# Performance work log

Measured on AMD Instinct MI355X. Metric: run time of the kernel, lower is better.

Reference implementation:

```python
import jax, jax.numpy as jnp
import numpy as np

N = 50000      # nodes
E = 500000     # edges (includes N self-loops)
DIN = 512
DOUT = 256
NEG_SLOPE = 0.01  # torch nn.LeakyReLU default


def setup_inputs() -> dict:
    key = jax.random.key(0)
    k1, k2, k3, k4, k5 = jax.random.split(key, 5)
    x = jax.random.normal(k1, (N, DIN), dtype=jnp.float32)
    # xavier_normal_ with gain=1.414
    std_W = 1.414 * np.sqrt(2.0 / (DIN + DOUT))
    W = jax.random.normal(k2, (DIN, DOUT), dtype=jnp.float32) * std_W
    std_a = 1.414 * np.sqrt(2.0 / (1 + 2 * DOUT))
    a = jax.random.normal(k3, (2 * DOUT,), dtype=jnp.float32) * std_a
    # first N edges are self-loops so every row-sum is nonzero
    loops = jnp.arange(N, dtype=jnp.int32)
    edge_src = jnp.concatenate([loops, jax.random.randint(k4, (E - N,), 0, N, dtype=jnp.int32)])
    edge_dst = jnp.concatenate([loops, jax.random.randint(k5, (E - N,), 0, N, dtype=jnp.int32)])
    return {"x": x, "W": W, "a": a, "edge_src": edge_src, "edge_dst": edge_dst}


def reference(x, W, a, edge_src, edge_dst):
    n = x.shape[0]
    d = W.shape[1]
    h = x @ W  # [N, DOUT]
    # a . [h_src ; h_dst] decomposed per-node, then gathered per-edge
    s_src = h @ a[:d]   # [N]
    s_dst = h @ a[d:]   # [N]
    score = s_src[edge_src] + s_dst[edge_dst]          # [E]
    e = jnp.exp(-jax.nn.leaky_relu(score, NEG_SLOPE))  # [E]
    # sparse softmax denominator: spmm(edge, e, ones) == segment sum over src
    e_rowsum = jax.ops.segment_sum(e, edge_src, num_segments=n)            # [N]
    # numerator: spmm(edge, e, h) == sum_j e_ij * h_j per row i
    h_prime = jax.ops.segment_sum(e[:, None] * h[edge_dst], edge_src, num_segments=n)  # [N, DOUT]
    h_prime = h_prime / e_rowsum[:, None]
    return jax.nn.elu(h_prime)  # concat=True branch
```

## Files before the change

kernel.cpp:

```cpp
#include <hip/hip_runtime.h>
#include <math.h>

#define DIN 512
#define DOUT 256
#define NEG_SLOPE 0.01f
#define BM 128
#define BK 32

typedef __attribute__((ext_vector_type(8))) short bf16x8;
typedef __attribute__((ext_vector_type(4))) float f32x4;
typedef __attribute__((ext_vector_type(4))) unsigned int u32x4;

__device__ __forceinline__ unsigned short f2bf(float f) {
    unsigned int u = __float_as_uint(f);
    unsigned int r = (u + 0x7FFFu + ((u >> 16) & 1u)) >> 16;
    return (unsigned short)r;
}
__device__ __forceinline__ float bf2f(unsigned short u) {
    return __uint_as_float(((unsigned int)u) << 16);
}
__device__ __forceinline__ unsigned int cvtpk(float lo, float hi) {
    unsigned int r;
    asm("v_cvt_pk_bf16_f32 %0, %1, %2" : "=v"(r) : "v"(lo), "v"(hi));
    return r;
}
__device__ __forceinline__ void gload16(const void* g, void* l) {
    __builtin_amdgcn_global_load_lds(
        (const __attribute__((address_space(1))) void*)g,
        (__attribute__((address_space(3))) void*)l, 16, 0, 0);
}

__global__ void wt_convert(const float* __restrict__ W, unsigned short* __restrict__ Wt) {
    int t = blockIdx.x * blockDim.x + threadIdx.x;
    if (t >= DIN * DOUT) return;
    int k = t >> 8;
    int c = t & 255;
    Wt[c * DIN + k] = f2bf(W[t]);
}

__global__ __launch_bounds__(512) void gemm_k(const float* __restrict__ x,
                                              const unsigned short* __restrict__ Wt,
                                              unsigned short* __restrict__ hb, int M) {
    __shared__ unsigned char lds[65536];
    const int t = threadIdx.x;
    const int lane = t & 63;
    const int wv = t >> 6;
    const int wr = wv >> 2;
    const int wc = wv & 3;
    const int m0 = blockIdx.x * BM;

    f32x4 acc[4][4] = {};

    auto stage = [&](int bb, int k0) {
#pragma unroll
        for (int ci = 0; ci < 4; ++ci) {
            int c = wv * 4 + ci;
            if (c < 16) {
                int row = c * 8 + (lane >> 3);
                int q = (lane & 7) ^ (lane >> 3);
                int rg = m0 + row; if (rg >= M) rg = M - 1;
                const float* src = x + (size_t)rg * DIN + k0 + q * 4;
                gload16(src, lds + bb * 16384 + c * 1024);
            } else {
                int cb = c - 16;
                int col = cb * 16 + (lane >> 2);
                int s = lane & 3;
                int sw = (col ^ (col >> 2)) & 3;
                int q8 = s ^ sw;
                const unsigned short* src = Wt + (size_t)col * DIN + k0 + q8 * 8;
                gload16(src, lds + 32768 + bb * 16384 + cb * 1024);
            }
        }
    };

    auto compute = [&](int bb) {
        const unsigned char* Ab = lds + bb * 16384;
        const unsigned char* Bb = lds + 32768 + bb * 16384;
        const int g = lane >> 4;
        bf16x8 af[4];
#pragma unroll
        for (int rf = 0; rf < 4; ++rf) {
            int row = wr * 64 + rf * 16 + (lane & 15);
            int r7 = row & 7;
            f32x4 v0 = *(const f32x4*)(Ab + row * 128 + (((2 * g) ^ r7) * 16));
            f32x4 v1 = *(const f32x4*)(Ab + row * 128 + (((2 * g + 1) ^ r7) * 16));
            u32x4 p;
            p.x = cvtpk(v0.x, v0.y);
            p.y = cvtpk(v0.z, v0.w);
            p.z = cvtpk(v1.x, v1.y);
            p.w = cvtpk(v1.z, v1.w);
            af[rf] = *(bf16x8*)&p;
        }
        bf16x8 bfr[4];
#pragma unroll
        for (int cf = 0; cf < 4; ++cf) {
            int col = wc * 64 + cf * 16 + (lane & 15);
            int sw = (col ^ (col >> 2)) & 3;
            bfr[cf] = *(const bf16x8*)(Bb + col * 64 + ((g ^ sw) * 16));
        }
#pragma unroll
        for (int rf = 0; rf < 4; ++rf)
#pragma unroll
            for (int cf = 0; cf < 4; ++cf)
                acc[rf][cf] = __builtin_amdgcn_mfma_f32_16x16x32_bf16(af[rf], bfr[cf], acc[rf][cf], 0, 0, 0);
    };

    stage(0, 0);
    for (int ts = 0; ts < DIN / BK; ++ts) {
        if (ts < DIN / BK - 1) stage((ts + 1) & 1, (ts + 1) * BK);
        __syncthreads();
        compute(ts & 1);
        __syncthreads();
    }

#pragma unroll
    for (int rf = 0; rf < 4; ++rf) {
#pragma unroll
        for (int j = 0; j < 4; ++j) {
            int row = m0 + wr * 64 + rf * 16 + (lane >> 4) * 4 + j;
            if (row < M) {
#pragma unroll
                for (int cf = 0; cf < 4; ++cf) {
                    int col = wc * 64 + cf * 16 + (lane & 15);
                    hb[(size_t)row * DOUT + col] = f2bf(acc[rf][cf][j]);
                }
            }
        }
    }
}

__global__ void node_scores(const unsigned short* __restrict__ hb, const float* __restrict__ a,
                            float* __restrict__ s_src, float* __restrict__ s_dst, int N) {
    int gt = blockIdx.x * blockDim.x + threadIdx.x;
    int w = gt >> 6;
    int lane = threadIdx.x & 63;
    if (w >= N) return;
    ushort4 hv = *(const ushort4*)(hb + (size_t)w * DOUT + lane * 4);
    float4 as = *(const float4*)(a + lane * 4);
    float4 ad = *(const float4*)(a + DOUT + lane * 4);
    float h0 = bf2f(hv.x), h1 = bf2f(hv.y), h2 = bf2f(hv.z), h3 = bf2f(hv.w);
    float ss = h0 * as.x + h1 * as.y + h2 * as.z + h3 * as.w;
    float sd = h0 * ad.x + h1 * ad.y + h2 * ad.z + h3 * ad.w;
#pragma unroll
    for (int off = 32; off > 0; off >>= 1) {
        ss += __shfl_xor(ss, off);
        sd += __shfl_xor(sd, off);
    }
    if (lane == 0) { s_src[w] = ss; s_dst[w] = sd; }
}

__global__ void zero_int(int* __restrict__ p, int n) {
    int i = blockIdx.x * blockDim.x + threadIdx.x;
    if (i < n) p[i] = 0;
}

__global__ void hist_k(const int* __restrict__ src, int* __restrict__ deg, int E) {
    int i = blockIdx.x * blockDim.x + threadIdx.x;
    if (i < E) atomicAdd(&deg[src[i]], 1);
}

__global__ __launch_bounds__(256) void block_sum(const int* __restrict__ deg, int* __restrict__ bsum, int N) {
    __shared__ int wsum[4];
    int b = blockIdx.x, t = threadIdx.x;
    int idx = b * 1024 + t * 4;
    int s = 0;
    if (idx + 3 < N) {
        int4 v = *(const int4*)(deg + idx);
        s = v.x + v.y + v.z + v.w;
    } else {
        for (int i = 0; i < 4; i++) if (idx + i < N) s += deg[idx + i];
    }
#pragma unroll
    for (int off = 32; off > 0; off >>= 1) s += __shfl_xor(s, off);
    if ((t & 63) == 0) wsum[t >> 6] = s;
    __syncthreads();
    if (t == 0) bsum[b] = wsum[0] + wsum[1] + wsum[2] + wsum[3];
}

__global__ void scan_tops(const int* __restrict__ bsum, int* __restrict__ boff,
                          int* __restrict__ rowptr, int nb, int N, int E) {
    int t = threadIdx.x;
    int v = (t < nb) ? bsum[t] : 0;
    int x = v;
#pragma unroll
    for (int off = 1; off < 64; off <<= 1) {
        int y = __shfl_up(x, off);
        if (t >= off) x += y;
    }
    if (t < nb) boff[t] = x - v;
    if (t == 0) rowptr[N] = E;
}

__global__ __launch_bounds__(256) void scan_blk(const int* __restrict__ deg, const int* __restrict__ boff,
                                                int* __restrict__ rowptr, int* __restrict__ cursor, int N) {
    __shared__ int wsum[4];
    int b = blockIdx.x, t = threadIdx.x;
    int idx = b * 1024 + t * 4;
    int v0 = 0, v1 = 0, v2 = 0, v3 = 0;
    if (idx + 3 < N) {
        int4 v = *(const int4*)(deg + idx);
        v0 = v.x; v1 = v.y; v2 = v.z; v3 = v.w;
    } else if (idx < N) {
        v0 = deg[idx];
        if (idx + 1 < N) v1 = deg[idx + 1];
        if (idx + 2 < N) v2 = deg[idx + 2];
    }
    int s = v0 + v1 + v2 + v3;
    int lane = t & 63, wid = t >> 6;
    int x = s;
#pragma unroll
    for (int off = 1; off < 64; off <<= 1) {
        int y = __shfl_up(x, off);
        if (lane >= off) x += y;
    }
    if (lane == 63) wsum[wid] = x;
    __syncthreads();
    int add = boff[b];
    for (int ww = 0; ww < wid; ++ww) add += wsum[ww];
    int e0 = add + x - s;
    int e1 = e0 + v0, e2 = e1 + v1, e3 = e2 + v2;
    if (idx < N)     { rowptr[idx] = e0;     cursor[idx] = e0; }
    if (idx + 1 < N) { rowptr[idx + 1] = e1; cursor[idx + 1] = e1; }
    if (idx + 2 < N) { rowptr[idx + 2] = e2; cursor[idx + 2] = e2; }
    if (idx + 3 < N) { rowptr[idx + 3] = e3; cursor[idx + 3] = e3; }
}

__global__ void edge_k(const int* __restrict__ src, const int* __restrict__ dst,
                       const float* __restrict__ s_src, const float* __restrict__ s_dst,
                       int* __restrict__ cursor, int2* __restrict__ csr, int E) {
    int i = blockIdx.x * blockDim.x + threadIdx.x;
    if (i >= E) return;
    int s = src[i], d = dst[i];
    float sc = s_src[s] + s_dst[d];
    float lrv = sc > 0.f ? sc : NEG_SLOPE * sc;
    float ev = __expf(-lrv);
    int pos = atomicAdd(&cursor[s], 1);
    csr[pos] = make_int2(d, __float_as_int(ev));
}

__global__ __launch_bounds__(256) void gather_k(const unsigned short* __restrict__ hb,
                                                const int* __restrict__ rowptr,
                                                const int2* __restrict__ csr,
                                                float* __restrict__ out, int N) {
    int gt = blockIdx.x * blockDim.x + threadIdx.x;
    int w = gt >> 6;
    int lane = threadIdx.x & 63;
    if (w >= N) return;
    int s0 = rowptr[w], s1 = rowptr[w + 1];
    float a0 = 0.f, a1 = 0.f, a2 = 0.f, a3 = 0.f, rs = 0.f;
    for (int base = s0; base < s1; base += 64) {
        int cnt = min(64, s1 - base);
        int dv = 0; float ev = 0.f;
        if (lane < cnt) {
            int2 p = csr[base + lane];
            dv = p.x; ev = __int_as_float(p.y);
        }
        int jj = 0;
        for (; jj + 4 <= cnt; jj += 4) {
            int d0 = __shfl(dv, jj), d1 = __shfl(dv, jj + 1), d2 = __shfl(dv, jj + 2), d3 = __shfl(dv, jj + 3);
            float e0 = __shfl(ev, jj), e1 = __shfl(ev, jj + 1), e2 = __shfl(ev, jj + 2), e3 = __shfl(ev, jj + 3);
            ushort4 h0 = *(const ushort4*)(hb + (size_t)d0 * DOUT + lane * 4);
            ushort4 h1 = *(const ushort4*)(hb + (size_t)d1 * DOUT + lane * 4);
            ushort4 h2 = *(const ushort4*)(hb + (size_t)d2 * DOUT + lane * 4);
            ushort4 h3 = *(const ushort4*)(hb + (size_t)d3 * DOUT + lane * 4);
            a0 += e0 * bf2f(h0.x) + e1 * bf2f(h1.x) + e2 * bf2f(h2.x) + e3 * bf2f(h3.x);
            a1 += e0 * bf2f(h0.y) + e1 * bf2f(h1.y) + e2 * bf2f(h2.y) + e3 * bf2f(h3.y);
            a2 += e0 * bf2f(h0.z) + e1 * bf2f(h1.z) + e2 * bf2f(h2.z) + e3 * bf2f(h3.z);
            a3 += e0 * bf2f(h0.w) + e1 * bf2f(h1.w) + e2 * bf2f(h2.w) + e3 * bf2f(h3.w);
            rs += e0 + e1 + e2 + e3;
        }
        for (; jj < cnt; ++jj) {
            int d0 = __shfl(dv, jj);
            float e0 = __shfl(ev, jj);
            ushort4 h0 = *(const ushort4*)(hb + (size_t)d0 * DOUT + lane * 4);
            a0 += e0 * bf2f(h0.x);
            a1 += e0 * bf2f(h0.y);
            a2 += e0 * bf2f(h0.z);
            a3 += e0 * bf2f(h0.w);
            rs += e0;
        }
    }
    float inv = 1.f / rs;
    float4 v;
    v.x = a0 * inv; v.y = a1 * inv; v.z = a2 * inv; v.w = a3 * inv;
    v.x = v.x > 0.f ? v.x : __expf(v.x) - 1.f;
    v.y = v.y > 0.f ? v.y : __expf(v.y) - 1.f;
    v.z = v.z > 0.f ? v.z : __expf(v.z) - 1.f;
    v.w = v.w > 0.f ? v.w : __expf(v.w) - 1.f;
    *(float4*)(out + (size_t)w * DOUT + lane * 4) = v;
}

extern "C" void kernel_launch(void* const* d_in, const int* in_sizes, int n_in,
                              void* d_out, int out_size, void* d_ws, size_t ws_size,
                              hipStream_t stream) {
    const float* x = (const float*)d_in[0];
    const float* W = (const float*)d_in[1];
    const float* a = (const float*)d_in[2];
    const int* edge_src = (const int*)d_in[3];
    const int* edge_dst = (const int*)d_in[4];

    const int N = in_sizes[0] / DIN;
    const int E = in_sizes[3];
    const int nb = (N + 1023) / 1024;

    char* ws = (char*)d_ws;
    size_t off = 0;
    auto alloc = [&](size_t bytes) {
        void* p = ws + off;
        off += (bytes + 15) & ~(size_t)15;
        return p;
    };
    unsigned short* hb = (unsigned short*)alloc((size_t)N * DOUT * 2);
    unsigned short* Wt = (unsigned short*)alloc((size_t)DIN * DOUT * 2);
    int* rowptr = (int*)alloc((size_t)(N + 1) * 4);
    int* deg = (int*)alloc((size_t)N * 4);
    int* cursor = (int*)alloc((size_t)N * 4);
    float* s_src = (float*)alloc((size_t)N * 4);
    float* s_dst = (float*)alloc((size_t)N * 4);
    int2* csr = (int2*)alloc((size_t)E * 8);
    int* bsum = (int*)alloc((size_t)nb * 4);
    int* boff = (int*)alloc((size_t)nb * 4);
    (void)ws_size;

    float* out = (float*)d_out;

    wt_convert<<<(DIN * DOUT + 255) / 256, 256, 0, stream>>>(W, Wt);
    gemm_k<<<(N + BM - 1) / BM, 512, 0, stream>>>(x, Wt, hb, N);
    zero_int<<<(N + 255) / 256, 256, 0, stream>>>(deg, N);
    node_scores<<<(N + 3) / 4, 256, 0, stream>>>(hb, a, s_src, s_dst, N);
    hist_k<<<(E + 255) / 256, 256, 0, stream>>>(edge_src, deg, E);
    block_sum<<<nb, 256, 0, stream>>>(deg, bsum, N);
    scan_tops<<<1, 64, 0, stream>>>(bsum, boff, rowptr, nb, N, E);
    scan_blk<<<nb, 256, 0, stream>>>(deg, boff, rowptr, cursor, N);
    edge_k<<<(E + 255) / 256, 256, 0, stream>>>(edge_src, edge_dst, s_src, s_dst,
                                                cursor, csr, E);
    gather_k<<<(N + 3) / 4, 256, 0, stream>>>(hb, rowptr, csr, out, N);
}
```

Measured before the change: 160.9 us.

## Restructure GEMM tiling, fuse node scores into epilogue, merge scan and prep kernels

The GEMM now tiles 256 rows by 64 columns over a 2D grid. Each block keeps its whole 64-column slice of W resident in LDS and streams x straight from global memory into registers, where it is converted to bf16. The node-score dot products are folded into the GEMM epilogue as partial sums added with atomics, which removes the node_scores pass that re-read h. The W transpose and the zeroing of deg and the scores are merged into one prep kernel, and the three-kernel scan becomes a single 1024-thread block. This cuts launches and the extra pass over h. The costs are float atomics on the scores, uncoalesced direct global A loads with no double buffering, and a serial single-block scan.

```diff
diff --git a/kernel.cpp b/kernel.cpp
--- a/kernel.cpp
+++ b/kernel.cpp
@@ -4,8 +4,8 @@
 #define DIN 512
 #define DOUT 256
 #define NEG_SLOPE 0.01f
-#define BM 128
-#define BK 32
+#define GBM 256
+#define GBN 64
 
 typedef __attribute__((ext_vector_type(8))) short bf16x8;
 typedef __attribute__((ext_vector_type(4))) float f32x4;
@@ -30,128 +30,110 @@
         (__attribute__((address_space(3))) void*)l, 16, 0, 0);
 }
 
-__global__ void wt_convert(const float* __restrict__ W, unsigned short* __restrict__ Wt) {
+__global__ void prep(const float* __restrict__ W, unsigned short* __restrict__ Wt,
+                     int* __restrict__ deg, float* __restrict__ s_src,
+                     float* __restrict__ s_dst, int N) {
     int t = blockIdx.x * blockDim.x + threadIdx.x;
-    if (t >= DIN * DOUT) return;
-    int k = t >> 8;
-    int c = t & 255;
-    Wt[c * DIN + k] = f2bf(W[t]);
+    if (t < DIN * DOUT) {
+        int k = t & (DIN - 1);
+        int c = t >> 9;
+        Wt[t] = f2bf(W[(size_t)k * DOUT + c]);
+    }
+    if (t < N) { deg[t] = 0; s_src[t] = 0.f; s_dst[t] = 0.f; }
 }
 
 __global__ __launch_bounds__(512) void gemm_k(const float* __restrict__ x,
                                               const unsigned short* __restrict__ Wt,
-                                              unsigned short* __restrict__ hb, int M) {
-    __shared__ unsigned char lds[65536];
+                                              unsigned short* __restrict__ hb,
+                                              const float* __restrict__ av,
+                                              float* __restrict__ s_src,
+                                              float* __restrict__ s_dst, int M) {
+    __shared__ unsigned char Bs[65536];
     const int t = threadIdx.x;
     const int lane = t & 63;
     const int wv = t >> 6;
-    const int wr = wv >> 2;
-    const int wc = wv & 3;
-    const int m0 = blockIdx.x * BM;
-
-    f32x4 acc[4][4] = {};
-
-    auto stage = [&](int bb, int k0) {
-#pragma unroll
-        for (int ci = 0; ci < 4; ++ci) {
-            int c = wv * 4 + ci;
-            if (c < 16) {
-                int row = c * 8 + (lane >> 3);
-                int q = (lane & 7) ^ (lane >> 3);
-                int rg = m0 + row; if (rg >= M) rg = M - 1;
-                const float* src = x + (size_t)rg * DIN + k0 + q * 4;
-                gload16(src, lds + bb * 16384 + c * 1024);
-            } else {
-                int cb = c - 16;
-                int col = cb * 16 + (lane >> 2);
-                int s = lane & 3;
-                int sw = (col ^ (col >> 2)) & 3;
-                int q8 = s ^ sw;
-                const unsigned short* src = Wt + (size_t)col * DIN + k0 + q8 * 8;
-                gload16(src, lds + 32768 + bb * 16384 + cb * 1024);
+    const int m0 = blockIdx.x * GBM;
+    const int n0 = blockIdx.y * GBN;
+
+#pragma unroll
+    for (int it = 0; it < 8; ++it) {
+        int c = wv * 8 + it;
+        const unsigned short* src = Wt + (size_t)(n0 + c) * DIN + ((lane ^ (c & 7)) * 8);
+        gload16(src, Bs + c * 1024);
+    }
+
+    float as_[4], ad_[4];
+#pragma unroll
+    for (int cf = 0; cf < 4; ++cf) {
+        int col = n0 + cf * 16 + (lane & 15);
+        as_[cf] = av[col];
+        ad_[cf] = av[DOUT + col];
+    }
+
+    f32x4 acc[2][4] = {};
+    const int g = lane >> 4;
+    int row0 = m0 + wv * 32 + (lane & 15);
+    int r0 = min(row0, M - 1);
+    int r1 = min(row0 + 16, M - 1);
+    const float* pA0 = x + (size_t)r0 * DIN + g * 8;
+    const float* pA1 = x + (size_t)r1 * DIN + g * 8;
+
+    __syncthreads();
+
+#pragma unroll 4
+    for (int ks = 0; ks < DIN / 32; ++ks) {
+        bf16x8 afr[2];
+        {
+            f32x4 v0 = *(const f32x4*)(pA0 + ks * 32);
+            f32x4 v1 = *(const f32x4*)(pA0 + ks * 32 + 4);
+            u32x4 p;
+            p.x = cvtpk(v0.x, v0.y); p.y = cvtpk(v0.z, v0.w);
+            p.z = cvtpk(v1.x, v1.y); p.w = cvtpk(v1.z, v1.w);
+            afr[0] = *(bf16x8*)&p;
+            f32x4 w0 = *(const f32x4*)(pA1 + ks * 32);
+            f32x4 w1 = *(const f32x4*)(pA1 + ks * 32 + 4);
+            u32x4 q;
+            q.x = cvtpk(w0.x, w0.y); q.y = cvtpk(w0.z, w0.w);
+            q.z = cvtpk(w1.x, w1.y); q.w = cvtpk(w1.z, w1.w);
+            afr[1] = *(bf16x8*)&q;
+        }
+#pragma unroll
+        for (int cf = 0; cf < 4; ++cf) {
+            int col = cf * 16 + (lane & 15);
+            bf16x8 bfr = *(const bf16x8*)(Bs + col * 1024 + (((ks * 4 + g) ^ (col & 7)) << 4));
+            acc[0][cf] = __builtin_amdgcn_mfma_f32_16x16x32_bf16(afr[0], bfr, acc[0][cf], 0, 0, 0);
+            acc[1][cf] = __builtin_amdgcn_mfma_f32_16x16x32_bf16(afr[1], bfr, acc[1][cf], 0, 0, 0);
+        }
+    }
+
+#pragma unroll
+    for (int rf = 0; rf < 2; ++rf) {
+#pragma unroll
+        for (int j = 0; j < 4; ++j) {
+            int row = m0 + wv * 32 + rf * 16 + g * 4 + j;
+            float ps = 0.f, pd = 0.f;
+#pragma unroll
+            for (int cf = 0; cf < 4; ++cf) {
+                float v = acc[rf][cf][j];
+                ps += v * as_[cf];
+                pd += v * ad_[cf];
             }
-        }
-    };
-
-    auto compute = [&](int bb) {
-        const unsigned char* Ab = lds + bb * 16384;
-        const unsigned char* Bb = lds + 32768 + bb * 16384;
-        const int g = lane >> 4;
-        bf16x8 af[4];
-#pragma unroll
-        for (int rf = 0; rf < 4; ++rf) {
-            int row = wr * 64 + rf * 16 + (lane & 15);
-            int r7 = row & 7;
-            f32x4 v0 = *(const f32x4*)(Ab + row * 128 + (((2 * g) ^ r7) * 16));
-            f32x4 v1 = *(const f32x4*)(Ab + row * 128 + (((2 * g + 1) ^ r7) * 16));
-            u32x4 p;
-            p.x = cvtpk(v0.x, v0.y);
-            p.y = cvtpk(v0.z, v0.w);
-            p.z = cvtpk(v1.x, v1.y);
-            p.w = cvtpk(v1.z, v1.w);
-            af[rf] = *(bf16x8*)&p;
-        }
-        bf16x8 bfr[4];
-#pragma unroll
-        for (int cf = 0; cf < 4; ++cf) {
-            int col = wc * 64 + cf * 16 + (lane & 15);
-            int sw = (col ^ (col >> 2)) & 3;
-            bfr[cf] = *(const bf16x8*)(Bb + col * 64 + ((g ^ sw) * 16));
-        }
-#pragma unroll
-        for (int rf = 0; rf < 4; ++rf)
-#pragma unroll
-            for (int cf = 0; cf < 4; ++cf)
-                acc[rf][cf] = __builtin_amdgcn_mfma_f32_16x16x32_bf16(af[rf], bfr[cf], acc[rf][cf], 0, 0, 0);
-    };
-
-    stage(0, 0);
-    for (int ts = 0; ts < DIN / BK; ++ts) {
-        if (ts < DIN / BK - 1) stage((ts + 1) & 1, (ts + 1) * BK);
-        __syncthreads();
-        compute(ts & 1);
-        __syncthreads();
-    }
-
-#pragma unroll
-    for (int rf = 0; rf < 4; ++rf) {
-#pragma unroll
-        for (int j = 0; j < 4; ++j) {
-            int row = m0 + wr * 64 + rf * 16 + (lane >> 4) * 4 + j;
+#pragma unroll
+            for (int off = 1; off < 16; off <<= 1) {
+                ps += __shfl_xor(ps, off);
+                pd += __shfl_xor(pd, off);
+            }
             if (row < M) {
 #pragma unroll
-                for (int cf = 0; cf < 4; ++cf) {
-                    int col = wc * 64 + cf * 16 + (lane & 15);
-                    hb[(size_t)row * DOUT + col] = f2bf(acc[rf][cf][j]);
+                for (int cf = 0; cf < 4; ++cf)
+                    hb[(size_t)row * DOUT + n0 + cf * 16 + (lane & 15)] = f2bf(acc[rf][cf][j]);
+                if ((lane & 15) == 0) {
+                    atomicAdd(&s_src[row], ps);
+                    atomicAdd(&s_dst[row], pd);
                 }
             }
         }
     }
-}
-
-__global__ void node_scores(const unsigned short* __restrict__ hb, const float* __restrict__ a,
-                            float* __restrict__ s_src, float* __restrict__ s_dst, int N) {
-    int gt = blockIdx.x * blockDim.x + threadIdx.x;
-    int w = gt >> 6;
-    int lane = threadIdx.x & 63;
-    if (w >= N) return;
-    ushort4 hv = *(const ushort4*)(hb + (size_t)w * DOUT + lane * 4);
-    float4 as = *(const float4*)(a + lane * 4);
-    float4 ad = *(const float4*)(a + DOUT + lane * 4);
-    float h0 = bf2f(hv.x), h1 = bf2f(hv.y), h2 = bf2f(hv.z), h3 = bf2f(hv.w);
-    float ss = h0 * as.x + h1 * as.y + h2 * as.z + h3 * as.w;
-    float sd = h0 * ad.x + h1 * ad.y + h2 * ad.z + h3 * ad.w;
-#pragma unroll
-    for (int off = 32; off > 0; off >>= 1) {
-        ss += __shfl_xor(ss, off);
-        sd += __shfl_xor(sd, off);
-    }
-    if (lane == 0) { s_src[w] = ss; s_dst[w] = sd; }
-}
-
-__global__ void zero_int(int* __restrict__ p, int n) {
-    int i = blockIdx.x * blockDim.x + threadIdx.x;
-    if (i < n) p[i] = 0;
 }
 
 __global__ void hist_k(const int* __restrict__ src, int* __restrict__ deg, int E) {
@@ -159,70 +141,39 @@
     if (i < E) atomicAdd(&deg[src[i]], 1);
 }
 
-__global__ __launch_bounds__(256) void block_sum(const int* __restrict__ deg, int* __restrict__ bsum, int N) {
-    __shared__ int wsum[4];
-    int b = blockIdx.x, t = threadIdx.x;
-    int idx = b * 1024 + t * 4;
+__global__ __launch_bounds__(1024) void scan_all(const int* __restrict__ deg,
+                                                 int* __restrict__ rowptr,
+                                                 int* __restrict__ cursor, int N, int E) {
+    __shared__ int wsum[16];
+    int t = threadIdx.x;
+    const int C = (N + 1023) >> 10;
+    int base = t * C;
     int s = 0;
-    if (idx + 3 < N) {
-        int4 v = *(const int4*)(deg + idx);
-        s = v.x + v.y + v.z + v.w;
-    } else {
-        for (int i = 0; i < 4; i++) if (idx + i < N) s += deg[idx + i];
-    }
-#pragma unroll
-    for (int off = 32; off > 0; off >>= 1) s += __shfl_xor(s, off);
-    if ((t & 63) == 0) wsum[t >> 6] = s;
+    for (int i = 0; i < C; ++i) {
+        int idx = base + i;
+        if (idx < N) s += deg[idx];
+    }
+    int lane = t & 63, wid = t >> 6;
+    int xx = s;
+#pragma unroll
+    for (int off = 1; off < 64; off <<= 1) {
+        int y = __shfl_up(xx, off);
+        if (lane >= off) xx += y;
+    }
+    if (lane == 63) wsum[wid] = xx;
     __syncthreads();
-    if (t == 0) bsum[b] = wsum[0] + wsum[1] + wsum[2] + wsum[3];
-}
-
-__global__ void scan_tops(const int* __restrict__ bsum, int* __restrict__ boff,
-                          int* __restrict__ rowptr, int nb, int N, int E) {
-    int t = threadIdx.x;
-    int v = (t < nb) ? bsum[t] : 0;
-    int x = v;
-#pragma unroll
-    for (int off = 1; off < 64; off <<= 1) {
-        int y = __shfl_up(x, off);
-        if (t >= off) x += y;
-    }
-    if (t < nb) boff[t] = x - v;
+    int add = 0;
+    for (int w = 0; w < wid; ++w) add += wsum[w];
+    int run = add + xx - s;
+    for (int i = 0; i < C; ++i) {
+        int idx = base + i;
+        if (idx < N) {
+            rowptr[idx] = run;
+            cursor[idx] = run;
+            run += deg[idx];
+        }
+    }
     if (t == 0) rowptr[N] = E;
-}
-
-__global__ __launch_bounds__(256) void scan_blk(const int* __restrict__ deg, const int* __restrict__ boff,
-                                                int* __restrict__ rowptr, int* __restrict__ cursor, int N) {
-    __shared__ int wsum[4];
-    int b = blockIdx.x, t = threadIdx.x;
-    int idx = b * 1024 + t * 4;
-    int v0 = 0, v1 = 0, v2 = 0, v3 = 0;
-    if (idx + 3 < N) {
-        int4 v = *(const int4*)(deg + idx);
-        v0 = v.x; v1 = v.y; v2 = v.z; v3 = v.w;
-    } else if (idx < N) {
-        v0 = deg[idx];
-        if (idx + 1 < N) v1 = deg[idx + 1];
-        if (idx + 2 < N) v2 = deg[idx + 2];
-    }
-    int s = v0 + v1 + v2 + v3;
-    int lane = t & 63, wid = t >> 6;
-    int x = s;
-#pragma unroll
-    for (int off = 1; off < 64; off <<= 1) {
-        int y = __shfl_up(x, off);
-        if (lane >= off) x += y;
-    }
-    if (lane == 63) wsum[wid] = x;
-    __syncthreads();
-    int add = boff[b];
-    for (int ww = 0; ww < wid; ++ww) add += wsum[ww];
-    int e0 = add + x - s;
-    int e1 = e0 + v0, e2 = e1 + v1, e3 = e2 + v2;
-    if (idx < N)     { rowptr[idx] = e0;     cursor[idx] = e0; }
-    if (idx + 1 < N) { rowptr[idx + 1] = e1; cursor[idx + 1] = e1; }
-    if (idx + 2 < N) { rowptr[idx + 2] = e2; cursor[idx + 2] = e2; }
-    if (idx + 3 < N) { rowptr[idx + 3] = e3; cursor[idx + 3] = e3; }
 }
 
 __global__ void edge_k(const int* __restrict__ src, const int* __restrict__ dst,
@@ -301,7 +252,6 @@
 
     const int N = in_sizes[0] / DIN;
     const int E = in_sizes[3];
-    const int nb = (N + 1023) / 1024;
 
     char* ws = (char*)d_ws;
     size_t off = 0;
@@ -318,20 +268,15 @@
     float* s_src = (float*)alloc((size_t)N * 4);
     float* s_dst = (float*)alloc((size_t)N * 4);
     int2* csr = (int2*)alloc((size_t)E * 8);
-    int* bsum = (int*)alloc((size_t)nb * 4);
-    int* boff = (int*)alloc((size_t)nb * 4);
     (void)ws_size;
 
     float* out = (float*)d_out;
 
-    wt_convert<<<(DIN * DOUT + 255) / 256, 256, 0, stream>>>(W, Wt);
-    gemm_k<<<(N + BM - 1) / BM, 512, 0, stream>>>(x, Wt, hb, N);
-    zero_int<<<(N + 255) / 256, 256, 0, stream>>>(deg, N);
-    node_scores<<<(N + 3) / 4, 256, 0, stream>>>(hb, a, s_src, s_dst, N);
+    prep<<<(DIN * DOUT + 255) / 256, 256, 0, stream>>>(W, Wt, deg, s_src, s_dst, N);
+    dim3 ggrid((N + GBM - 1) / GBM, DOUT / GBN);
+    gemm_k<<<ggrid, 512, 0, stream>>>(x, Wt, hb, a, s_src, s_dst, N);
     hist_k<<<(E + 255) / 256, 256, 0, stream>>>(edge_src, deg, E);
-    block_sum<<<nb, 256, 0, stream>>>(deg, bsum, N);
-    scan_tops<<<1, 64, 0, stream>>>(bsum, boff, rowptr, nb, N, E);
-    scan_blk<<<nb, 256, 0, stream>>>(deg, boff, rowptr, cursor, N);
+    scan_all<<<1, 1024, 0, stream>>>(deg, rowptr, cursor, N, E);
     edge_k<<<(E + 255) / 256, 256, 0, stream>>>(edge_src, edge_dst, s_src, s_dst,
                                                 cursor, csr, E);
     gather_k<<<(N + 3) / 4, 256, 0, stream>>>(hb, rowptr, csr, out, N);
```

Result: slower. 291.8 us (+81.4%).
